# Optimization experiments

Measured on AMD Instinct MI355X. Metric: run time of the kernel, lower is better.

The kernel has to match this reference:

```python
import jax, jax.numpy as jnp
import numpy as np

# irreps_in = irreps_out = 32x0e + 16x1o ; irreps_sh = 1x0e + 1x1o
MUL0, MUL1 = 32, 16
N_NODES = 12000
N_EDGES = 120000
INV_SQRT3 = float(1.0 / np.sqrt(3.0))   # w3j(1,1,0), w3j(0,1,1), w3j(1,0,1) coefficient
SQRT2 = float(np.sqrt(2.0))             # e3nn normalize2mom constant for ReLU
# e3nn TP norms: irrep_normalization='component', path_normalization='element'.
# Each output irrep receives paths with num_elements 32 and 16 -> x = 48.
N_0E = float(1.0 / np.sqrt(48.0))       # alpha = dim(0e)/48 = 1/48
N_1O = float(np.sqrt(3.0 / 48.0))       # alpha = dim(1o)/48 = 3/48
# uvw weight blocks (mul2 = 1): (s,y0->s),(s,y0->g),(v,y1->s),(v,y1->g),(s,y1->v),(v,y0->v)
SPLITS = [MUL0 * MUL0, MUL0 * MUL1, MUL1 * MUL0, MUL1 * MUL1, MUL0 * MUL1, MUL1 * MUL1]
OFFS = np.cumsum([0] + SPLITS)
WNUM = int(OFFS[-1])  # 3072


def setup_inputs() -> dict:
    key = jax.random.key(0)
    k1, k2, k3, k4, k5 = jax.random.split(key, 5)
    x = jax.random.normal(k1, (N_NODES, MUL0 + 3 * MUL1), dtype=jnp.float32)
    edge_attr = jax.random.normal(k2, (N_EDGES, 64), dtype=jnp.float32)
    Yij = jax.random.normal(k3, (N_EDGES, 4), dtype=jnp.float32)
    edge_index = jax.random.randint(k4, (2, N_EDGES), 0, N_NODES, dtype=jnp.int64)
    w_emb = jax.random.normal(k5, (2 * MUL0 + 64, WNUM), dtype=jnp.float32)
    return {"x": x, "edge_attr": edge_attr, "Yij": Yij,
            "edge_index": edge_index, "w_emb": w_emb}


def reference(x, edge_attr, Yij, edge_index, w_emb):
    dst, src = edge_index[0], edge_index[1]
    E = edge_attr.shape[0]
    xs = x[:, :MUL0]                                   # [N, 32] scalars (0e)
    xv = x[:, MUL0:].reshape(-1, MUL1, 3)              # [N, 16, 3] vectors (1o)

    # per-edge weight MLP (single e3nn FC layer, weight scaled by 1/sqrt(fan_in))
    emb = jnp.concatenate([xs[dst], xs[src], edge_attr], axis=-1)     # [E, 128]
    w = emb @ (w_emb / np.sqrt(w_emb.shape[0]))                       # [E, 3072]
    Ws = [w[:, OFFS[i]:OFFS[i + 1]] for i in range(6)]
    W1 = Ws[0].reshape(E, MUL0, MUL0)
    W2 = Ws[1].reshape(E, MUL0, MUL1)
    W3 = Ws[2].reshape(E, MUL1, MUL0)
    W4 = Ws[3].reshape(E, MUL1, MUL1)
    W5 = Ws[4].reshape(E, MUL0, MUL1)
    W6 = Ws[5].reshape(E, MUL1, MUL1)

    # gather source features, split sh
    x1s, x1v = xs[src], xv[src]                        # [E,32], [E,16,3]
    y0, y1 = Yij[:, 0], Yij[:, 1:4]                    # [E], [E,3]

    sy0 = x1s * y0[:, None]                            # 0e x 0e paths
    vdot = jnp.einsum('euk,ek->eu', x1v, y1) * INV_SQRT3  # 1o x 1o -> 0e
    out_s = N_0E * (jnp.einsum('euw,eu->ew', W1, sy0) +
                    jnp.einsum('euw,eu->ew', W3, vdot))    # [E, 32]
    out_g = N_0E * (jnp.einsum('euw,eu->ew', W2, sy0) +
                    jnp.einsum('euw,eu->ew', W4, vdot))    # [E, 16]
    out_v = (N_1O * INV_SQRT3) * (
        jnp.einsum('euw,eu,ek->ewk', W5, x1s, y1) +
        jnp.einsum('euw,euk->ewk', W6, x1v * y0[:, None, None]))  # [E, 16, 3]

    msg = jnp.concatenate([out_s, out_g, out_v.reshape(E, MUL1 * 3)], axis=-1)  # [E, 96]

    # scatter mean onto destination nodes
    summed = jax.ops.segment_sum(msg, dst, num_segments=N_NODES)
    cnt = jax.ops.segment_sum(jnp.ones((E,), msg.dtype), dst, num_segments=N_NODES)
    mean = summed / jnp.maximum(cnt, 1.0)[:, None]

    # Gate (e3nn Activation normalizes ReLU by sqrt(2))
    s = SQRT2 * jax.nn.relu(mean[:, :MUL0])
    g = SQRT2 * jax.nn.relu(mean[:, MUL0:MUL0 + MUL1])
    v = mean[:, MUL0 + MUL1:].reshape(-1, MUL1, 3) * g[:, :, None]
    out = jnp.concatenate([s, v.reshape(-1, MUL1 * 3)], axis=-1)     # [N, 80]
    return x + out
```

## Files before the change

### kernel.cpp

```cpp
#include <hip/hip_runtime.h>
#include <hip/hip_bf16.h>

#define E_EDGES 120000
#define NUM_NODES 12000

typedef __attribute__((ext_vector_type(8))) short bfrag;
typedef __attribute__((ext_vector_type(8))) unsigned short ushort8;
typedef __attribute__((ext_vector_type(4))) float f32x4;

#define INV_SQRT3 0.57735026918962576f
#define SQRT2_C   1.41421356237309515f
#define N_0E_C    0.14433756729740643f
#define NV_C      0.14433756729740643f
#define WSCALE    0.08838834764831845f

__device__ __forceinline__ unsigned short f2bf(float f) {
    union { float f; unsigned int u; } v; v.f = f;
    unsigned int r = v.u + 0x7fffu + ((v.u >> 16) & 1u);
    return (unsigned short)(r >> 16);
}

__device__ __forceinline__ ushort8 pack8(f32x4 a, f32x4 b) {
    ushort8 o;
    o[0] = f2bf(a.x); o[1] = f2bf(a.y); o[2] = f2bf(a.z); o[3] = f2bf(a.w);
    o[4] = f2bf(b.x); o[5] = f2bf(b.y); o[6] = f2bf(b.z); o[7] = f2bf(b.w);
    return o;
}

__global__ void k_wt(const float* __restrict__ w_emb, unsigned short* __restrict__ Bt) {
    int o = blockIdx.x * 256 + threadIdx.x;
    if (o >= 3072 * 128) return;
    int t = o >> 11;
    int c = (o >> 3) & 255;
    int j = o & 7;
    int kb = c >> 6;
    int quad = (c >> 4) & 3;
    int col = c & 15;
    int k = kb * 32 + quad * 8 + j;
    int n = t * 16 + col;
    Bt[o] = f2bf(w_emb[k * 3072 + n] * WSCALE);
}

__global__ void k_prep(const float* __restrict__ x, const float* __restrict__ edge_attr,
                       const float* __restrict__ Yij, const int* __restrict__ edge_index,
                       unsigned short* __restrict__ emb, float* __restrict__ rT,
                       float* __restrict__ cnt) {
    int e = blockIdx.x * 256 + threadIdx.x;
    if (e >= E_EDGES) return;
    int dst = edge_index[e];
    int src = edge_index[E_EDGES + e];
    f32x4 y = *(const f32x4*)(Yij + 4 * (long)e);
    float y0 = y.x, y1a = y.y, y1b = y.z, y1c = y.w;
    const float* xd = x + (long)dst * 80;
    const float* xs = x + (long)src * 80;
    const float* ea = edge_attr + (long)e * 64;

    ushort8* embp = (ushort8*)(emb + (long)e * 128);

    float xsv[80];
#pragma unroll
    for (int i = 0; i < 80; i += 4) {
        f32x4 v = *(const f32x4*)(xs + i);
        xsv[i] = v.x; xsv[i + 1] = v.y; xsv[i + 2] = v.z; xsv[i + 3] = v.w;
    }
#pragma unroll
    for (int cb = 0; cb < 4; ++cb) {
        f32x4 a = *(const f32x4*)(xd + cb * 8);
        f32x4 b = *(const f32x4*)(xd + cb * 8 + 4);
        embp[cb] = pack8(a, b);
    }
#pragma unroll
    for (int cb = 0; cb < 4; ++cb) {
        f32x4 a, b;
        a.x = xsv[cb * 8 + 0]; a.y = xsv[cb * 8 + 1]; a.z = xsv[cb * 8 + 2]; a.w = xsv[cb * 8 + 3];
        b.x = xsv[cb * 8 + 4]; b.y = xsv[cb * 8 + 5]; b.z = xsv[cb * 8 + 6]; b.w = xsv[cb * 8 + 7];
        embp[4 + cb] = pack8(a, b);
    }
#pragma unroll
    for (int cb = 0; cb < 8; ++cb) {
        f32x4 a = *(const f32x4*)(ea + cb * 8);
        f32x4 b = *(const f32x4*)(ea + cb * 8 + 4);
        embp[8 + cb] = pack8(a, b);
    }
#pragma unroll
    for (int u = 0; u < 32; ++u) rT[(long)u * E_EDGES + e] = xsv[u] * y0;
#pragma unroll
    for (int u = 0; u < 16; ++u)
        rT[(long)(32 + u) * E_EDGES + e] =
            (xsv[32 + 3 * u] * y1a + xsv[33 + 3 * u] * y1b + xsv[34 + 3 * u] * y1c) * INV_SQRT3;
#pragma unroll
    for (int u = 0; u < 32; ++u) rT[(long)(48 + u) * E_EDGES + e] = xsv[u];
#pragma unroll
    for (int j = 0; j < 48; ++j) rT[(long)(80 + j) * E_EDGES + e] = xsv[32 + j] * y0;
    atomicAdd(cnt + dst, 1.0f);
}

__global__ __launch_bounds__(256, 4) void k_gemm(
    const unsigned short* __restrict__ emb, const unsigned short* __restrict__ Bt,
    const float* __restrict__ rT, const int* __restrict__ edge_index,
    const float* __restrict__ Yij, float* __restrict__ summed) {
    const int lane = threadIdx.x & 63;
    const int wave = threadIdx.x >> 6;
    long e0 = (long)blockIdx.x * 128 + (long)wave * 32;
    const bool dup = (e0 + 32 > E_EDGES);
    if (dup) e0 = E_EDGES - 32;
    const int col = lane & 15, quad = lane >> 4;

    __shared__ __align__(16) char lds[2][16384];

    bfrag A[2][4];
#pragma unroll
    for (int s = 0; s < 2; ++s) {
        const unsigned short* ap = emb + (e0 + s * 16 + col) * 128 + quad * 8;
#pragma unroll
        for (int kb = 0; kb < 4; ++kb) A[s][kb] = *(const bfrag*)(ap + kb * 32);
    }

    auto stage = [&](int ci) {
        const char* g = (const char*)Bt + (size_t)ci * 16384 + wave * 4096 + lane * 16;
        char* l = &lds[ci & 1][wave * 4096];
#pragma unroll
        for (int j = 0; j < 4; ++j)
            __builtin_amdgcn_global_load_lds(
                (const __attribute__((address_space(1))) unsigned int*)(g + j * 1024),
                (__attribute__((address_space(3))) unsigned int*)(l + j * 1024), 16, 0, 0);
    };

    f32x4 z = {0.f, 0.f, 0.f, 0.f};
    f32x4 acc_s0[2] = {z, z}, acc_s1[2] = {z, z}, acc_g[2] = {z, z}, acc_t5[2] = {z, z};
    f32x4 acc_v[2][3] = {{z, z, z}, {z, z, z}};

    const float* rbase = rT + e0 + quad * 4;
    auto loadw = [&](int r, f32x4& a, f32x4& b) {
        const float* p = rbase + (long)r * E_EDGES;
        a = *(const f32x4*)(p);
        b = *(const f32x4*)(p + 16);
    };

    auto tile = [&](const char* lt, f32x4& c0, f32x4& c1) {
        bfrag B0 = *(const bfrag*)(lt + lane * 16);
        bfrag B1 = *(const bfrag*)(lt + lane * 16 + 1024);
        bfrag B2 = *(const bfrag*)(lt + lane * 16 + 2048);
        bfrag B3 = *(const bfrag*)(lt + lane * 16 + 3072);
        c0 = z; c1 = z;
        c0 = __builtin_amdgcn_mfma_f32_16x16x32_bf16(A[0][0], B0, c0, 0, 0, 0);
        c1 = __builtin_amdgcn_mfma_f32_16x16x32_bf16(A[1][0], B0, c1, 0, 0, 0);
        c0 = __builtin_amdgcn_mfma_f32_16x16x32_bf16(A[0][1], B1, c0, 0, 0, 0);
        c1 = __builtin_amdgcn_mfma_f32_16x16x32_bf16(A[1][1], B1, c1, 0, 0, 0);
        c0 = __builtin_amdgcn_mfma_f32_16x16x32_bf16(A[0][2], B2, c0, 0, 0, 0);
        c1 = __builtin_amdgcn_mfma_f32_16x16x32_bf16(A[1][2], B2, c1, 0, 0, 0);
        c0 = __builtin_amdgcn_mfma_f32_16x16x32_bf16(A[0][3], B3, c0, 0, 0, 0);
        c1 = __builtin_amdgcn_mfma_f32_16x16x32_bf16(A[1][3], B3, c1, 0, 0, 0);
    };

    stage(0);
    int cidx = 0;
    auto nextbuf = [&]() -> const char* {
        __syncthreads();
        if (cidx + 1 < 48) stage(cidx + 1);
        const char* b = lds[cidx & 1];
        ++cidx;
        return b;
    };

    f32x4 c0, c1;

    {
        f32x4 p0a, p0b, p1a, p1b;
        loadw(0, p0a, p0b); loadw(1, p1a, p1b);
#pragma unroll 1
        for (int j = 0; j < 16; ++j) {
            const char* buf = nextbuf();
            f32x4 w0a = p0a, w0b = p0b, w1a = p1a, w1b = p1b;
            int nr = (j < 15) ? (2 * j + 2) : 0;
            loadw(nr, p0a, p0b); loadw(nr + 1, p1a, p1b);
            tile(buf,         c0, c1); acc_s0[0] += c0 * w0a; acc_s0[1] += c1 * w0b;
            tile(buf + 4096,  c0, c1); acc_s1[0] += c0 * w0a; acc_s1[1] += c1 * w0b;
            tile(buf + 8192,  c0, c1); acc_s0[0] += c0 * w1a; acc_s0[1] += c1 * w1b;
            tile(buf + 12288, c0, c1); acc_s1[0] += c0 * w1a; acc_s1[1] += c1 * w1b;
        }
    }
    {
        f32x4 pa[4], pb[4];
#pragma unroll
        for (int i = 0; i < 4; ++i) loadw(i, pa[i], pb[i]);
#pragma unroll 1
        for (int j = 0; j < 8; ++j) {
            const char* buf = nextbuf();
            f32x4 wa[4], wb[4];
#pragma unroll
            for (int i = 0; i < 4; ++i) { wa[i] = pa[i]; wb[i] = pb[i]; }
            int nr = (j < 7) ? (4 * j + 4) : 0;
#pragma unroll
            for (int i = 0; i < 4; ++i) loadw(nr + i, pa[i], pb[i]);
#pragma unroll
            for (int i = 0; i < 4; ++i) {
                tile(buf + i * 4096, c0, c1);
                acc_g[0] += c0 * wa[i]; acc_g[1] += c1 * wb[i];
            }
        }
    }
    {
        f32x4 p0a, p0b, p1a, p1b;
        loadw(32, p0a, p0b); loadw(33, p1a, p1b);
#pragma unroll 1
        for (int j = 0; j < 8; ++j) {
            const char* buf = nextbuf();
            f32x4 w0a = p0a, w0b = p0b, w1a = p1a, w1b = p1b;
            int nr = (j < 7) ? (32 + 2 * j + 2) : 32;
            loadw(nr, p0a, p0b); loadw(nr + 1, p1a, p1b);
            tile(buf,         c0, c1); acc_s0[0] += c0 * w0a; acc_s0[1] += c1 * w0b;
            tile(buf + 4096,  c0, c1); acc_s1[0] += c0 * w0a; acc_s1[1] += c1 * w0b;
            tile(buf + 8192,  c0, c1); acc_s0[0] += c0 * w1a; acc_s0[1] += c1 * w1b;
            tile(buf + 12288, c0, c1); acc_s1[0] += c0 * w1a; acc_s1[1] += c1 * w1b;
        }
    }
    {
        f32x4 pa[4], pb[4];
#pragma unroll
        for (int i = 0; i < 4; ++i) loadw(32 + i, pa[i], pb[i]);
#pragma unroll 1
        for (int j = 0; j < 4; ++j) {
            const char* buf = nextbuf();
            f32x4 wa[4], wb[4];
#pragma unroll
            for (int i = 0; i < 4; ++i) { wa[i] = pa[i]; wb[i] = pb[i]; }
            int nr = (j < 3) ? (32 + 4 * j + 4) : 32;
#pragma unroll
            for (int i = 0; i < 4; ++i) loadw(nr + i, pa[i], pb[i]);
#pragma unroll
            for (int i = 0; i < 4; ++i) {
                tile(buf + i * 4096, c0, c1);
                acc_g[0] += c0 * wa[i]; acc_g[1] += c1 * wb[i];
            }
        }
    }
    {
        f32x4 pa[4], pb[4];
#pragma unroll
        for (int i = 0; i < 4; ++i) loadw(48 + i, pa[i], pb[i]);
#pragma unroll 1
        for (int j = 0; j < 8; ++j) {
            const char* buf = nextbuf();
            f32x4 wa[4], wb[4];
#pragma unroll
            for (int i = 0; i < 4; ++i) { wa[i] = pa[i]; wb[i] = pb[i]; }
            int nr = (j < 7) ? (48 + 4 * j + 4) : 48;
#pragma unroll
            for (int i = 0; i < 4; ++i) loadw(nr + i, pa[i], pb[i]);
#pragma unroll
            for (int i = 0; i < 4; ++i) {
                tile(buf + i * 4096, c0, c1);
                acc_t5[0] += c0 * wa[i]; acc_t5[1] += c1 * wb[i];
            }
        }
    }
    {
        f32x4 va[3], vb[3];
#pragma unroll
        for (int k = 0; k < 3; ++k) loadw(80 + k, va[k], vb[k]);
#pragma unroll 1
        for (int j = 0; j < 4; ++j) {
            const char* buf = nextbuf();
#pragma unroll
            for (int i = 0; i < 4; ++i) {
                f32x4 wa[3], wb[3];
#pragma unroll
                for (int k = 0; k < 3; ++k) { wa[k] = va[k]; wb[k] = vb[k]; }
                int un = 4 * j + i + 1; if (un > 15) un = 0;
#pragma unroll
                for (int k = 0; k < 3; ++k) loadw(80 + 3 * un + k, va[k], vb[k]);
                tile(buf + i * 4096, c0, c1);
#pragma unroll
                for (int k = 0; k < 3; ++k) {
                    acc_v[0][k] += c0 * wa[k];
                    acc_v[1][k] += c1 * wb[k];
                }
            }
        }
    }

    if (dup) return;
#pragma unroll
    for (int s = 0; s < 2; ++s) {
        long eb = e0 + s * 16 + quad * 4;
#pragma unroll
        for (int r = 0; r < 4; ++r) {
            long e = eb + r;
            int d = edge_index[e];
            float* base = summed + (long)d * 96;
            float y1a = Yij[4 * e + 1], y1b = Yij[4 * e + 2], y1c = Yij[4 * e + 3];
            atomicAdd(base + col,       N_0E_C * acc_s0[s][r]);
            atomicAdd(base + col + 16,  N_0E_C * acc_s1[s][r]);
            atomicAdd(base + 32 + col,  N_0E_C * acc_g[s][r]);
            float t5 = acc_t5[s][r];
            atomicAdd(base + 48 + col * 3 + 0, NV_C * (t5 * y1a + acc_v[s][0][r]));
            atomicAdd(base + 48 + col * 3 + 1, NV_C * (t5 * y1b + acc_v[s][1][r]));
            atomicAdd(base + 48 + col * 3 + 2, NV_C * (t5 * y1c + acc_v[s][2][r]));
        }
    }
}

__global__ void k_final(const float* __restrict__ x, const float* __restrict__ summed,
                        const float* __restrict__ cnt, float* __restrict__ out) {
    int tid = blockIdx.x * 256 + threadIdx.x;
    if (tid >= NUM_NODES * 80) return;
    int n = tid / 80, c = tid % 80;
    float m = fmaxf(cnt[n], 1.0f);
    float inv = 1.0f / m;
    float val;
    if (c < 32) {
        val = SQRT2_C * fmaxf(summed[(long)n * 96 + c] * inv, 0.0f);
    } else {
        int j = c - 32;
        int w = j / 3;
        float g = SQRT2_C * fmaxf(summed[(long)n * 96 + 32 + w] * inv, 0.0f);
        val = summed[(long)n * 96 + 48 + j] * inv * g;
    }
    out[tid] = x[tid] + val;
}

extern "C" void kernel_launch(void* const* d_in, const int* in_sizes, int n_in,
                              void* d_out, int out_size, void* d_ws, size_t ws_size,
                              hipStream_t stream) {
    const float* x         = (const float*)d_in[0];
    const float* edge_attr = (const float*)d_in[1];
    const float* Yij       = (const float*)d_in[2];
    const int*   edge_index= (const int*)d_in[3];
    const float* w_emb     = (const float*)d_in[4];
    float* out = (float*)d_out;

    char* ws = (char*)d_ws;
    size_t off = 0;
    unsigned short* emb = (unsigned short*)(ws + off); off += (size_t)E_EDGES * 128 * 2;
    unsigned short* Bt  = (unsigned short*)(ws + off); off += (size_t)3072 * 128 * 2;
    off = (off + 255) & ~(size_t)255;
    float* rT     = (float*)(ws + off); off += (size_t)128 * E_EDGES * 4;
    size_t zoff = off;
    float* summed = (float*)(ws + off); off += (size_t)NUM_NODES * 96 * 4;
    float* cnt    = (float*)(ws + off); off += (size_t)NUM_NODES * 4;

    hipMemsetAsync(ws + zoff, 0, (size_t)NUM_NODES * 97 * 4, stream);
    k_wt  <<<(3072 * 128 + 255) / 256, 256, 0, stream>>>(w_emb, Bt);
    k_prep<<<(E_EDGES + 255) / 256, 256, 0, stream>>>(x, edge_attr, Yij, edge_index, emb, rT, cnt);
    k_gemm<<<(E_EDGES + 127) / 128, 256, 0, stream>>>(emb, Bt, rT, edge_index, Yij, summed);
    k_final<<<(NUM_NODES * 80 + 255) / 256, 256, 0, stream>>>(x, summed, cnt, out);
}
```

Before: 299.3 us.

## Replace atomic scatter-mean with CSR sort by destination and per-node reduction

Builds a CSR grouping of edges by destination node (count, scan, scatter permutation). The GEMM kernel now writes per-edge messages with plain stores instead of float atomics, and a per-node kernel sums the messages and applies the mean and gate. The aim is to remove atomic contention on the summed buffer, at the cost of an extra 46 MB message buffer round trip, three small extra launches and a single-block scan.

```diff
diff --git a/kernel.cpp b/kernel.cpp
--- a/kernel.cpp
+++ b/kernel.cpp
@@ -41,10 +41,44 @@
     Bt[o] = f2bf(w_emb[k * 3072 + n] * WSCALE);
 }
 
+__global__ void k_count(const int* __restrict__ edge_index, int* __restrict__ cnt) {
+    int e = blockIdx.x * 256 + threadIdx.x;
+    if (e >= E_EDGES) return;
+    atomicAdd(cnt + edge_index[e], 1);
+}
+
+__global__ void k_scan(const int* __restrict__ cnt, int* __restrict__ offs) {
+    __shared__ int psum[256];
+    int t = threadIdx.x;
+    const int SEG = (NUM_NODES + 255) / 256;
+    int lo = t * SEG;
+    int hi = lo + SEG; if (hi > NUM_NODES) hi = NUM_NODES;
+    int s = 0;
+    for (int i = lo; i < hi; ++i) s += cnt[i];
+    psum[t] = s;
+    __syncthreads();
+    if (t == 0) {
+        int acc = 0;
+        for (int i = 0; i < 256; ++i) { int v = psum[i]; psum[i] = acc; acc += v; }
+    }
+    __syncthreads();
+    int acc = psum[t];
+    for (int i = lo; i < hi; ++i) { offs[i] = acc; acc += cnt[i]; }
+    if (t == 255) offs[NUM_NODES] = acc;
+}
+
+__global__ void k_scatter(const int* __restrict__ edge_index, const int* __restrict__ offs,
+                          int* __restrict__ cursor, int* __restrict__ perm_src) {
+    int e = blockIdx.x * 256 + threadIdx.x;
+    if (e >= E_EDGES) return;
+    int d = edge_index[e];
+    int p = offs[d] + atomicAdd(cursor + d, 1);
+    perm_src[p] = e;
+}
+
 __global__ void k_prep(const float* __restrict__ x, const float* __restrict__ edge_attr,
                        const float* __restrict__ Yij, const int* __restrict__ edge_index,
-                       unsigned short* __restrict__ emb, float* __restrict__ rT,
-                       float* __restrict__ cnt) {
+                       unsigned short* __restrict__ emb, float* __restrict__ rT) {
     int e = blockIdx.x * 256 + threadIdx.x;
     if (e >= E_EDGES) return;
     int dst = edge_index[e];
@@ -92,13 +126,12 @@
     for (int u = 0; u < 32; ++u) rT[(long)(48 + u) * E_EDGES + e] = xsv[u];
 #pragma unroll
     for (int j = 0; j < 48; ++j) rT[(long)(80 + j) * E_EDGES + e] = xsv[32 + j] * y0;
-    atomicAdd(cnt + dst, 1.0f);
 }
 
 __global__ __launch_bounds__(256, 4) void k_gemm(
     const unsigned short* __restrict__ emb, const unsigned short* __restrict__ Bt,
-    const float* __restrict__ rT, const int* __restrict__ edge_index,
-    const float* __restrict__ Yij, float* __restrict__ summed) {
+    const float* __restrict__ rT, const float* __restrict__ Yij,
+    float* __restrict__ msg) {
     const int lane = threadIdx.x & 63;
     const int wave = threadIdx.x >> 6;
     long e0 = (long)blockIdx.x * 128 + (long)wave * 32;
@@ -287,37 +320,49 @@
 #pragma unroll
         for (int r = 0; r < 4; ++r) {
             long e = eb + r;
-            int d = edge_index[e];
-            float* base = summed + (long)d * 96;
+            float* base = msg + e * 96;
             float y1a = Yij[4 * e + 1], y1b = Yij[4 * e + 2], y1c = Yij[4 * e + 3];
-            atomicAdd(base + col,       N_0E_C * acc_s0[s][r]);
-            atomicAdd(base + col + 16,  N_0E_C * acc_s1[s][r]);
-            atomicAdd(base + 32 + col,  N_0E_C * acc_g[s][r]);
+            base[col]            = N_0E_C * acc_s0[s][r];
+            base[col + 16]       = N_0E_C * acc_s1[s][r];
+            base[32 + col]       = N_0E_C * acc_g[s][r];
             float t5 = acc_t5[s][r];
-            atomicAdd(base + 48 + col * 3 + 0, NV_C * (t5 * y1a + acc_v[s][0][r]));
-            atomicAdd(base + 48 + col * 3 + 1, NV_C * (t5 * y1b + acc_v[s][1][r]));
-            atomicAdd(base + 48 + col * 3 + 2, NV_C * (t5 * y1c + acc_v[s][2][r]));
-        }
-    }
-}
-
-__global__ void k_final(const float* __restrict__ x, const float* __restrict__ summed,
-                        const float* __restrict__ cnt, float* __restrict__ out) {
-    int tid = blockIdx.x * 256 + threadIdx.x;
-    if (tid >= NUM_NODES * 80) return;
-    int n = tid / 80, c = tid % 80;
-    float m = fmaxf(cnt[n], 1.0f);
-    float inv = 1.0f / m;
-    float val;
-    if (c < 32) {
-        val = SQRT2_C * fmaxf(summed[(long)n * 96 + c] * inv, 0.0f);
-    } else {
-        int j = c - 32;
-        int w = j / 3;
-        float g = SQRT2_C * fmaxf(summed[(long)n * 96 + 32 + w] * inv, 0.0f);
-        val = summed[(long)n * 96 + 48 + j] * inv * g;
-    }
-    out[tid] = x[tid] + val;
+            base[48 + col * 3 + 0] = NV_C * (t5 * y1a + acc_v[s][0][r]);
+            base[48 + col * 3 + 1] = NV_C * (t5 * y1b + acc_v[s][1][r]);
+            base[48 + col * 3 + 2] = NV_C * (t5 * y1c + acc_v[s][2][r]);
+        }
+    }
+}
+
+__global__ __launch_bounds__(128) void k_nodesum(
+    const float* __restrict__ msg, const int* __restrict__ perm_src,
+    const int* __restrict__ offs, const float* __restrict__ x,
+    float* __restrict__ out) {
+    int n = blockIdx.x;
+    int t = threadIdx.x;
+    int lo = offs[n], hi = offs[n + 1];
+    float s = 0.0f;
+    if (t < 96) {
+        for (int i = lo; i < hi; ++i) {
+            int p = perm_src[i];
+            s += msg[(long)p * 96 + t];
+        }
+    }
+    float inv = 1.0f / fmaxf((float)(hi - lo), 1.0f);
+    __shared__ float sm[96];
+    if (t < 96) sm[t] = s * inv;
+    __syncthreads();
+    if (t < 80) {
+        float val;
+        if (t < 32) {
+            val = SQRT2_C * fmaxf(sm[t], 0.0f);
+        } else {
+            int j = t - 32;
+            int w = j / 3;
+            float g = SQRT2_C * fmaxf(sm[32 + w], 0.0f);
+            val = sm[48 + j] * g;
+        }
+        out[(long)n * 80 + t] = x[(long)n * 80 + t] + val;
+    }
 }
 
 extern "C" void kernel_launch(void* const* d_in, const int* in_sizes, int n_in,
@@ -335,14 +380,20 @@
     unsigned short* emb = (unsigned short*)(ws + off); off += (size_t)E_EDGES * 128 * 2;
     unsigned short* Bt  = (unsigned short*)(ws + off); off += (size_t)3072 * 128 * 2;
     off = (off + 255) & ~(size_t)255;
-    float* rT     = (float*)(ws + off); off += (size_t)128 * E_EDGES * 4;
+    float* rT      = (float*)(ws + off); off += (size_t)128 * E_EDGES * 4;
+    float* msg     = (float*)(ws + off); off += (size_t)E_EDGES * 96 * 4;
+    int*   perm_src= (int*)(ws + off);   off += (size_t)E_EDGES * 4;
+    int*   offs    = (int*)(ws + off);   off += (size_t)(NUM_NODES + 1) * 4;
     size_t zoff = off;
-    float* summed = (float*)(ws + off); off += (size_t)NUM_NODES * 96 * 4;
-    float* cnt    = (float*)(ws + off); off += (size_t)NUM_NODES * 4;
-
-    hipMemsetAsync(ws + zoff, 0, (size_t)NUM_NODES * 97 * 4, stream);
-    k_wt  <<<(3072 * 128 + 255) / 256, 256, 0, stream>>>(w_emb, Bt);
-    k_prep<<<(E_EDGES + 255) / 256, 256, 0, stream>>>(x, edge_attr, Yij, edge_index, emb, rT, cnt);
-    k_gemm<<<(E_EDGES + 127) / 128, 256, 0, stream>>>(emb, Bt, rT, edge_index, Yij, summed);
-    k_final<<<(NUM_NODES * 80 + 255) / 256, 256, 0, stream>>>(x, summed, cnt, out);
-}
+    int*   cnt     = (int*)(ws + off);   off += (size_t)NUM_NODES * 4;
+    int*   cursor  = (int*)(ws + off);   off += (size_t)NUM_NODES * 4;
+
+    hipMemsetAsync(ws + zoff, 0, (size_t)NUM_NODES * 2 * 4, stream);
+    k_wt     <<<(3072 * 128 + 255) / 256, 256, 0, stream>>>(w_emb, Bt);
+    k_count  <<<(E_EDGES + 255) / 256, 256, 0, stream>>>(edge_index, cnt);
+    k_scan   <<<1, 256, 0, stream>>>(cnt, offs);
+    k_scatter<<<(E_EDGES + 255) / 256, 256, 0, stream>>>(edge_index, offs, cursor, perm_src);
+    k_prep   <<<(E_EDGES + 255) / 256, 256, 0, stream>>>(x, edge_attr, Yij, edge_index, emb, rT);
+    k_gemm   <<<(E_EDGES + 127) / 128, 256, 0, stream>>>(emb, Bt, rT, Yij, msg);
+    k_nodesum<<<NUM_NODES, 128, 0, stream>>>(msg, perm_src, offs, x, out);
+}
```

After: 336.9 us. 12.6% more time.
